# Performance work log

Hardware: AMD Instinct MI355X
Metric: run time of the kernel (lower is better)

Reference implementation:

```python
import jax, jax.numpy as jnp
import numpy as np

HIDDEN = 1024
HEADS = 16
HEAD_DIM = HIDDEN // HEADS
SCALE = HEAD_DIM ** (-0.5)


def setup_inputs() -> dict:
    key = jax.random.key(0)
    ks = jax.random.split(key, 5)
    B, N, C = 8, 1024, HIDDEN
    x = jax.random.normal(ks[0], (B, N, C), dtype=jnp.float32)
    # torch nn.Linear params: weight [out, in], bias [out]
    w_in = jax.random.normal(ks[1], (3 * C, C), dtype=jnp.float32) * (C ** -0.5)
    b_in = jax.random.normal(ks[2], (3 * C,), dtype=jnp.float32) * 0.02
    w_out = jax.random.normal(ks[3], (C, C), dtype=jnp.float32) * (C ** -0.5)
    b_out = jax.random.normal(ks[4], (C,), dtype=jnp.float32) * 0.02
    return {"x": x, "w_in": w_in, "b_in": b_in, "w_out": w_out, "b_out": b_out}


def reference(x, w_in, b_in, w_out, b_out):
    B, N, C = x.shape
    H, D = HEADS, HEAD_DIM
    # in_proj: [B,N,3C] -> (3,B,H,N,D)
    qkv = x @ w_in.T + b_in
    qkv = qkv.reshape(B, N, 3, H, D).transpose(2, 0, 3, 1, 4)
    q, k, v = qkv[0], qkv[1], qkv[2]
    # attention scores scaled after QK^T (same math as scaling q)
    attn = jnp.einsum("bhnd,bhmd->bhnm", q, k) * SCALE
    attn = jax.nn.softmax(attn, axis=-1)
    out = jnp.einsum("bhnm,bhmd->bhnd", attn, v)  # [B,H,N,D]
    out = out.transpose(0, 2, 1, 3).reshape(B, N, C)
    return out @ w_out.T + b_out
```

## Files before the change

kernel.cpp:

```cpp
#include <hip/hip_runtime.h>


typedef __attribute__((ext_vector_type(8))) __bf16 bf16x8;
typedef __attribute__((ext_vector_type(4))) __bf16 bf16x4;
typedef __attribute__((ext_vector_type(4))) float f32x4;
typedef __attribute__((ext_vector_type(4))) short short4v;

__device__ __forceinline__ f32x4 mfma16(bf16x8 a, bf16x8 b, f32x4 c) {
  return __builtin_amdgcn_mfma_f32_16x16x32_bf16(a, b, c, 0, 0, 0);
}

#if __has_builtin(__builtin_amdgcn_mfma_f32_16x16x16bf16_1k)
__device__ __forceinline__ f32x4 mfma_pv(bf16x4 a, bf16x4 b, f32x4 c) {
  short4v as = __builtin_bit_cast(short4v, a);
  short4v bs = __builtin_bit_cast(short4v, b);
  return __builtin_amdgcn_mfma_f32_16x16x16bf16_1k(as, bs, c, 0, 0, 0);
}
#else
__device__ __forceinline__ f32x4 mfma_pv(bf16x4 a, bf16x4 b, f32x4 c) {
  __bf16 z = (__bf16)0.f;
  bf16x8 a8 = {a[0], a[1], a[2], a[3], z, z, z, z};
  bf16x8 b8 = {b[0], b[1], b[2], b[3], z, z, z, z};
  return mfma16(a8, b8, c);
}
#endif

__device__ __forceinline__ float fexp2(float x) {
#if __has_builtin(__builtin_amdgcn_exp2f)
  return __builtin_amdgcn_exp2f(x);
#else
  return exp2f(x);
#endif
}

typedef __attribute__((address_space(1))) const unsigned int gu32;
typedef __attribute__((address_space(3))) unsigned int lu32;

__device__ __forceinline__ void async16(const void* g, void* l) {
  __builtin_amdgcn_global_load_lds((gu32*)g, (lu32*)l, 16, 0, 0);
}

__global__ __launch_bounds__(256) void cvt_all(const float* __restrict__ x,
                                               __bf16* __restrict__ xb,
                                               const float* __restrict__ wi,
                                               __bf16* __restrict__ wib,
                                               const float* __restrict__ wo,
                                               __bf16* __restrict__ wob) {
  int blk = blockIdx.x;
  const float* in;
  __bf16* out;
  int base;
  if (blk < 4096)      { in = x;  out = xb;  base = 0; }
  else if (blk < 5632) { in = wi; out = wib; base = 4096; }
  else                 { in = wo; out = wob; base = 5632; }
  int i = ((blk - base) * 256 + threadIdx.x) * 8;
  float4 a = *(const float4*)(in + i);
  float4 b = *(const float4*)(in + i + 4);
  bf16x8 o;
  o[0] = (__bf16)a.x; o[1] = (__bf16)a.y; o[2] = (__bf16)a.z; o[3] = (__bf16)a.w;
  o[4] = (__bf16)b.x; o[5] = (__bf16)b.y; o[6] = (__bf16)b.z; o[7] = (__bf16)b.w;
  *(bf16x8*)(out + i) = o;
}

template <bool WRITE_VT>
__global__ __launch_bounds__(512, 4) void gemm1(const __bf16* __restrict__ A,
                                                const __bf16* __restrict__ Bm,
                                                const float* __restrict__ bias,
                                                __bf16* __restrict__ C,
                                                __bf16* __restrict__ vt) {
  __shared__ char lds[49152];
  const int t = threadIdx.x;
  const int wv = t >> 6, lane = t & 63;
  const int q16 = lane & 15, quad = lane >> 4;
  const int wm = wv >> 1, wn = wv & 1;
  const int bid = blockIdx.x;
  const long m0 = (long)(bid & 31) * 256;
  const long n0 = (long)(bid >> 5) * 128;

  const int sr4 = t >> 2;
  const int gc = (t & 3) ^ ((sr4 >> 1) & 3);
  const int ldst = wv * 1024;

  const __bf16* srcA0 = A + (m0 + sr4) * 1024 + gc * 8;
  const __bf16* srcA1 = A + (m0 + 128 + sr4) * 1024 + gc * 8;
  const __bf16* srcB  = Bm + (n0 + sr4) * 1024 + gc * 8;

  const int raB = (wm * 64 + q16) * 64 + ((quad ^ ((q16 >> 1) & 3)) * 16);
  const int rbB = (wn * 64 + q16) * 64 + ((quad ^ ((q16 >> 1) & 3)) * 16);

  f32x4 zero = {0.f, 0.f, 0.f, 0.f};
  f32x4 acc[4][4];
#pragma unroll
  for (int i = 0; i < 4; ++i)
#pragma unroll
    for (int j = 0; j < 4; ++j) acc[i][j] = zero;

  async16(srcA0, lds + ldst);
  async16(srcA1, lds + 8192 + ldst);
  async16(srcB, lds + 16384 + ldst);
  __syncthreads();

  int cur = 0;
#pragma unroll 1
  for (int t32 = 0; t32 < 32; ++t32) {
    char* Ac = lds + cur * 24576;
    char* Bc = Ac + 16384;

    if (t32 < 31) {
      char* S = lds + (cur ^ 1) * 24576;
      const int kt = (t32 + 1) * 32;
      async16(srcA0 + kt, S + ldst);
      async16(srcA1 + kt, S + 8192 + ldst);
      async16(srcB + kt, S + 16384 + ldst);
    }

    bf16x8 af[4], bfr[4];
#pragma unroll
    for (int mi = 0; mi < 4; ++mi)
      af[mi] = *(const bf16x8*)(Ac + raB + mi * 1024);
#pragma unroll
    for (int nj = 0; nj < 4; ++nj)
      bfr[nj] = *(const bf16x8*)(Bc + rbB + nj * 1024);

    __builtin_amdgcn_s_setprio(1);
#pragma unroll
    for (int mi = 0; mi < 4; ++mi)
#pragma unroll
      for (int nj = 0; nj < 4; ++nj)
        acc[mi][nj] = mfma16(af[mi], bfr[nj], acc[mi][nj]);
    __builtin_amdgcn_s_setprio(0);

    __syncthreads();
    cur ^= 1;
  }

  if (WRITE_VT && n0 >= 2048) {
    const int b = (int)(m0 >> 10);
    const int nbase = (int)(m0 & 1023) + wm * 64;
#pragma unroll
    for (int nj = 0; nj < 4; ++nj) {
      int col = (int)n0 + wn * 64 + nj * 16 + q16;
      int cc = col - 2048;
      int h = cc >> 6, d = cc & 63;
      float bs = bias[col];
      __bf16* vrow = vt + (((long)(b * 16 + h)) << 16) + (long)d * 1024;
#pragma unroll
      for (int mi = 0; mi < 4; ++mi) {
        int n = nbase + mi * 16 + quad * 4;
        bf16x4 o;
#pragma unroll
        for (int r = 0; r < 4; ++r) o[r] = (__bf16)(acc[mi][nj][r] + bs);
        *(bf16x4*)(vrow + n) = o;
      }
    }
  } else {
#pragma unroll
    for (int nj = 0; nj < 4; ++nj) {
      long col = n0 + wn * 64 + nj * 16 + q16;
      float bs = bias[col];
#pragma unroll
      for (int mi = 0; mi < 4; ++mi) {
        long rowb = m0 + wm * 64 + mi * 16 + quad * 4;
#pragma unroll
        for (int r = 0; r < 4; ++r) {
          float v = acc[mi][nj][r] + bs;
          C[(rowb + r) * 3072 + col] = (__bf16)v;
        }
      }
    }
  }
}

__global__ __launch_bounds__(256, 4) void gemm2(const __bf16* __restrict__ A,
                                                const __bf16* __restrict__ Bm,
                                                const float* __restrict__ bias,
                                                float* __restrict__ C) {
  __shared__ char lds[32768];
  const int t = threadIdx.x;
  const int wv = t >> 6, lane = t & 63;
  const int q16 = lane & 15, quad = lane >> 4;
  const int wm = wv >> 1, wn = wv & 1;
  const long m0 = (long)blockIdx.x * 128;
  const long n0 = (long)blockIdx.y * 128;

  const int sr4 = t >> 2;
  const int gc = (t & 3) ^ ((sr4 >> 1) & 3);
  const int ldst = wv * 1024;

  const __bf16* srcA0 = A + (m0 + sr4) * 1024 + gc * 8;
  const __bf16* srcA1 = A + (m0 + 64 + sr4) * 1024 + gc * 8;
  const __bf16* srcB0 = Bm + (n0 + sr4) * 1024 + gc * 8;
  const __bf16* srcB1 = Bm + (n0 + 64 + sr4) * 1024 + gc * 8;

  const int raB = (wm * 64 + q16) * 64 + ((quad ^ ((q16 >> 1) & 3)) * 16);
  const int rbB = (wn * 64 + q16) * 64 + ((quad ^ ((q16 >> 1) & 3)) * 16);

  f32x4 zero = {0.f, 0.f, 0.f, 0.f};
  f32x4 acc[4][4];
#pragma unroll
  for (int i = 0; i < 4; ++i)
#pragma unroll
    for (int j = 0; j < 4; ++j) acc[i][j] = zero;

  async16(srcA0, lds + ldst);
  async16(srcA1, lds + 4096 + ldst);
  async16(srcB0, lds + 8192 + ldst);
  async16(srcB1, lds + 12288 + ldst);
  __syncthreads();

  int cur = 0;
#pragma unroll 1
  for (int t32 = 0; t32 < 32; ++t32) {
    char* Ac = lds + cur * 16384;
    char* Bc = Ac + 8192;

    if (t32 < 31) {
      char* S = lds + (cur ^ 1) * 16384;
      const int kt = (t32 + 1) * 32;
      async16(srcA0 + kt, S + ldst);
      async16(srcA1 + kt, S + 4096 + ldst);
      async16(srcB0 + kt, S + 8192 + ldst);
      async16(srcB1 + kt, S + 12288 + ldst);
    }

    bf16x8 af[4], bfr[4];
#pragma unroll
    for (int mi = 0; mi < 4; ++mi)
      af[mi] = *(const bf16x8*)(Ac + raB + mi * 1024);
#pragma unroll
    for (int nj = 0; nj < 4; ++nj)
      bfr[nj] = *(const bf16x8*)(Bc + rbB + nj * 1024);

    __builtin_amdgcn_s_setprio(1);
#pragma unroll
    for (int mi = 0; mi < 4; ++mi)
#pragma unroll
      for (int nj = 0; nj < 4; ++nj)
        acc[mi][nj] = mfma16(af[mi], bfr[nj], acc[mi][nj]);
    __builtin_amdgcn_s_setprio(0);

    __syncthreads();
    cur ^= 1;
  }

#pragma unroll
  for (int nj = 0; nj < 4; ++nj) {
    long col = n0 + wn * 64 + nj * 16 + q16;
    float bs = bias[col];
#pragma unroll
    for (int mi = 0; mi < 4; ++mi) {
      long rowb = m0 + wm * 64 + mi * 16 + quad * 4;
#pragma unroll
      for (int r = 0; r < 4; ++r) {
        float v = acc[mi][nj][r] + bs;
        C[(rowb + r) * 1024 + col] = v;
      }
    }
  }
}

__global__ __launch_bounds__(256) void attn_kernel(const __bf16* __restrict__ qkv,
                                                   const __bf16* __restrict__ vt,
                                                   __bf16* __restrict__ ao) {
  __shared__ __bf16 Ks[64 * 64];
  __shared__ __bf16 Vt[64 * 64];
  const int t = threadIdx.x;
  const int wv = t >> 6, lane = t & 63;
  const int q16 = lane & 15, quad = lane >> 4;
  const int bh = blockIdx.x;
  const int b = bh >> 4, h = bh & 15;
  const int q0 = blockIdx.y * 64;
  const long rowbase = (long)b * 1024;

  bf16x8 qf0, qf1;
  {
    long qrow = rowbase + q0 + wv * 16 + q16;
    const __bf16* qp = qkv + qrow * 3072 + h * 64 + quad * 8;
    qf0 = *(const bf16x8*)qp;
    qf1 = *(const bf16x8*)(qp + 32);
#pragma unroll
    for (int j = 0; j < 8; ++j) {
      qf0[j] = (__bf16)((float)qf0[j] * 0.18033688f);
      qf1[j] = (__bf16)((float)qf1[j] * 0.18033688f);
    }
  }

  f32x4 zero = {0.f, 0.f, 0.f, 0.f};
  f32x4 oacc[4];
#pragma unroll
  for (int dt = 0; dt < 4; ++dt) oacc[dt] = zero;
  float lcol = 0.f;

  char* KsB = (char*)Ks;
  char* VtB = (char*)Vt;
  const int sr = t >> 3;
  const int sgc = (t & 7) ^ (sr & 7);
  const int sw = q16 & 7;

  for (int kv0 = 0; kv0 < 1024; kv0 += 64) {
    __syncthreads();
    const __bf16* kg = qkv + (rowbase + kv0 + sr) * 3072 + 1024 + h * 64 + sgc * 8;
    async16(kg, KsB + wv * 1024);
    async16(kg + (long)32 * 3072, KsB + 4096 + wv * 1024);
    const __bf16* vg = vt + (long)bh * 65536 + (long)sr * 1024 + kv0 + sgc * 8;
    async16(vg, VtB + wv * 1024);
    async16(vg + (long)32 * 1024, VtB + 4096 + wv * 1024);
    __syncthreads();

    f32x4 sacc[4];
#pragma unroll
    for (int nt = 0; nt < 4; ++nt) sacc[nt] = zero;
#pragma unroll
    for (int nt = 0; nt < 4; ++nt) {
      int kvr = nt * 16 + q16;
      bf16x8 kf0 = *(const bf16x8*)(KsB + kvr * 128 + ((quad ^ sw) * 16));
      bf16x8 kf1 = *(const bf16x8*)(KsB + kvr * 128 + (((4 + quad) ^ sw) * 16));
      sacc[nt] = mfma16(kf0, qf0, sacc[nt]);
      sacc[nt] = mfma16(kf1, qf1, sacc[nt]);
    }

    bf16x4 pf[4];
#pragma unroll
    for (int nt = 0; nt < 4; ++nt)
#pragma unroll
      for (int r = 0; r < 4; ++r) {
        float p = fexp2(sacc[nt][r]);
        lcol += p;
        pf[nt][r] = (__bf16)p;
      }

#pragma unroll
    for (int nt = 0; nt < 4; ++nt) {
      int c = ((nt * 2 + (quad >> 1)) ^ sw) * 16 + (quad & 1) * 8;
#pragma unroll
      for (int dt = 0; dt < 4; ++dt) {
        bf16x4 vf = *(const bf16x4*)(VtB + (dt * 16 + q16) * 128 + c);
        oacc[dt] = mfma_pv(pf[nt], vf, oacc[dt]);
      }
    }
  }

  lcol += __shfl_xor(lcol, 16);
  lcol += __shfl_xor(lcol, 32);
  float inv = 1.0f / lcol;
#pragma unroll
  for (int r = 0; r < 4; ++r) {
    float ir = __shfl(inv, quad * 4 + r);
    long orow = rowbase + q0 + wv * 16 + quad * 4 + r;
#pragma unroll
    for (int dt = 0; dt < 4; ++dt)
      ao[orow * 1024 + h * 64 + dt * 16 + q16] = (__bf16)(oacc[dt][r] * ir);
  }
}

extern "C" void kernel_launch(void* const* d_in, const int* in_sizes, int n_in,
                              void* d_out, int out_size, void* d_ws, size_t ws_size,
                              hipStream_t stream) {
  const float* x     = (const float*)d_in[0];
  const float* w_in  = (const float*)d_in[1];
  const float* b_in  = (const float*)d_in[2];
  const float* w_out = (const float*)d_in[3];
  const float* b_out = (const float*)d_in[4];
  float* out = (float*)d_out;

  char* ws = (char*)d_ws;
  __bf16* xb   = (__bf16*)(ws);
  __bf16* wib  = (__bf16*)(ws + 16777216);
  __bf16* wob  = (__bf16*)(ws + 23068672);
  __bf16* qkvb = (__bf16*)(ws + 25165824);
  __bf16* aob  = (__bf16*)(ws + 75497472);
  __bf16* vtg  = (__bf16*)d_out;

  cvt_all<<<6144, 256, 0, stream>>>(x, xb, w_in, wib, w_out, wob);
  gemm1<true><<<768, 512, 0, stream>>>(xb, wib, b_in, qkvb, vtg);
  attn_kernel<<<dim3(128, 16), 256, 0, stream>>>(qkvb, vtg, aob);
  gemm2<<<dim3(64, 8), 256, 0, stream>>>(aob, wob, b_out, out);
}
```

Baseline: 237.6 us.

## Double-buffer attention KV tiles and shrink out-projection GEMM M-tile

The attention kernel moves from a single-buffered 64-row K/V tile, loaded between two barriers, to a double-buffered 32-row tile. The next tile's async loads now overlap the current tile's QK and PV MFMAs, leaving one barrier per iteration. The output-projection GEMM cuts its M tile from 128 to 64 rows, doubling its grid to 1024 blocks for better CU occupancy. The cost is more loop iterations with smaller MFMA batches and less operand reuse per block.

New measurement: 242.3 us. Within noise of the previous version (+2.0%).

```diff
diff --git a/kernel.cpp b/kernel.cpp
--- a/kernel.cpp
+++ b/kernel.cpp
@@ -175,57 +175,54 @@
                                                 const __bf16* __restrict__ Bm,
                                                 const float* __restrict__ bias,
                                                 float* __restrict__ C) {
-  __shared__ char lds[32768];
+  __shared__ char lds[24576];
   const int t = threadIdx.x;
   const int wv = t >> 6, lane = t & 63;
   const int q16 = lane & 15, quad = lane >> 4;
   const int wm = wv >> 1, wn = wv & 1;
-  const long m0 = (long)blockIdx.x * 128;
+  const long m0 = (long)blockIdx.x * 64;
   const long n0 = (long)blockIdx.y * 128;
 
-  const int sr4 = t >> 2;
-  const int gc = (t & 3) ^ ((sr4 >> 1) & 3);
+  const int sr2 = t >> 2;
+  const int gc = (t & 3) ^ ((sr2 >> 1) & 3);
   const int ldst = wv * 1024;
 
-  const __bf16* srcA0 = A + (m0 + sr4) * 1024 + gc * 8;
-  const __bf16* srcA1 = A + (m0 + 64 + sr4) * 1024 + gc * 8;
-  const __bf16* srcB0 = Bm + (n0 + sr4) * 1024 + gc * 8;
-  const __bf16* srcB1 = Bm + (n0 + 64 + sr4) * 1024 + gc * 8;
-
-  const int raB = (wm * 64 + q16) * 64 + ((quad ^ ((q16 >> 1) & 3)) * 16);
+  const __bf16* srcA  = A + (m0 + sr2) * 1024 + gc * 8;
+  const __bf16* srcB0 = Bm + (n0 + sr2) * 1024 + gc * 8;
+  const __bf16* srcB1 = Bm + (n0 + 64 + sr2) * 1024 + gc * 8;
+
+  const int raB = (wm * 32 + q16) * 64 + ((quad ^ ((q16 >> 1) & 3)) * 16);
   const int rbB = (wn * 64 + q16) * 64 + ((quad ^ ((q16 >> 1) & 3)) * 16);
 
   f32x4 zero = {0.f, 0.f, 0.f, 0.f};
-  f32x4 acc[4][4];
-#pragma unroll
-  for (int i = 0; i < 4; ++i)
+  f32x4 acc[2][4];
+#pragma unroll
+  for (int i = 0; i < 2; ++i)
 #pragma unroll
     for (int j = 0; j < 4; ++j) acc[i][j] = zero;
 
-  async16(srcA0, lds + ldst);
-  async16(srcA1, lds + 4096 + ldst);
-  async16(srcB0, lds + 8192 + ldst);
-  async16(srcB1, lds + 12288 + ldst);
+  async16(srcA, lds + ldst);
+  async16(srcB0, lds + 4096 + ldst);
+  async16(srcB1, lds + 8192 + ldst);
   __syncthreads();
 
   int cur = 0;
 #pragma unroll 1
   for (int t32 = 0; t32 < 32; ++t32) {
-    char* Ac = lds + cur * 16384;
-    char* Bc = Ac + 8192;
+    char* Ac = lds + cur * 12288;
+    char* Bc = Ac + 4096;
 
     if (t32 < 31) {
-      char* S = lds + (cur ^ 1) * 16384;
+      char* S = lds + (cur ^ 1) * 12288;
       const int kt = (t32 + 1) * 32;
-      async16(srcA0 + kt, S + ldst);
-      async16(srcA1 + kt, S + 4096 + ldst);
-      async16(srcB0 + kt, S + 8192 + ldst);
-      async16(srcB1 + kt, S + 12288 + ldst);
-    }
-
-    bf16x8 af[4], bfr[4];
-#pragma unroll
-    for (int mi = 0; mi < 4; ++mi)
+      async16(srcA + kt, S + ldst);
+      async16(srcB0 + kt, S + 4096 + ldst);
+      async16(srcB1 + kt, S + 8192 + ldst);
+    }
+
+    bf16x8 af[2], bfr[4];
+#pragma unroll
+    for (int mi = 0; mi < 2; ++mi)
       af[mi] = *(const bf16x8*)(Ac + raB + mi * 1024);
 #pragma unroll
     for (int nj = 0; nj < 4; ++nj)
@@ -233,7 +230,7 @@
 
     __builtin_amdgcn_s_setprio(1);
 #pragma unroll
-    for (int mi = 0; mi < 4; ++mi)
+    for (int mi = 0; mi < 2; ++mi)
 #pragma unroll
       for (int nj = 0; nj < 4; ++nj)
         acc[mi][nj] = mfma16(af[mi], bfr[nj], acc[mi][nj]);
@@ -248,8 +245,8 @@
     long col = n0 + wn * 64 + nj * 16 + q16;
     float bs = bias[col];
 #pragma unroll
-    for (int mi = 0; mi < 4; ++mi) {
-      long rowb = m0 + wm * 64 + mi * 16 + quad * 4;
+    for (int mi = 0; mi < 2; ++mi) {
+      long rowb = m0 + wm * 32 + mi * 16 + quad * 4;
 #pragma unroll
       for (int r = 0; r < 4; ++r) {
         float v = acc[mi][nj][r] + bs;
@@ -262,8 +259,7 @@
 __global__ __launch_bounds__(256) void attn_kernel(const __bf16* __restrict__ qkv,
                                                    const __bf16* __restrict__ vt,
                                                    __bf16* __restrict__ ao) {
-  __shared__ __bf16 Ks[64 * 64];
-  __shared__ __bf16 Vt[64 * 64];
+  __shared__ char lds[16384];
   const int t = threadIdx.x;
   const int wv = t >> 6, lane = t & 63;
   const int q16 = lane & 15, quad = lane >> 4;
@@ -291,27 +287,39 @@
   for (int dt = 0; dt < 4; ++dt) oacc[dt] = zero;
   float lcol = 0.f;
 
-  char* KsB = (char*)Ks;
-  char* VtB = (char*)Vt;
-  const int sr = t >> 3;
-  const int sgc = (t & 7) ^ (sr & 7);
+  const int sr8 = t >> 3;
+  const int sgc8 = (t & 7) ^ (sr8 & 7);
+  const int sr2 = t >> 2;
+  const int gc4 = (t & 3) ^ ((sr2 >> 1) & 3);
+  const int ldst = wv * 1024;
+
+  const __bf16* kbase = qkv + (rowbase + sr8) * 3072 + 1024 + h * 64 + sgc8 * 8;
+  const __bf16* vbase = vt + (long)bh * 65536 + (long)sr2 * 1024 + gc4 * 8;
+
   const int sw = q16 & 7;
-
-  for (int kv0 = 0; kv0 < 1024; kv0 += 64) {
-    __syncthreads();
-    const __bf16* kg = qkv + (rowbase + kv0 + sr) * 3072 + 1024 + h * 64 + sgc * 8;
-    async16(kg, KsB + wv * 1024);
-    async16(kg + (long)32 * 3072, KsB + 4096 + wv * 1024);
-    const __bf16* vg = vt + (long)bh * 65536 + (long)sr * 1024 + kv0 + sgc * 8;
-    async16(vg, VtB + wv * 1024);
-    async16(vg + (long)32 * 1024, VtB + 4096 + wv * 1024);
-    __syncthreads();
-
-    f32x4 sacc[4];
-#pragma unroll
-    for (int nt = 0; nt < 4; ++nt) sacc[nt] = zero;
-#pragma unroll
-    for (int nt = 0; nt < 4; ++nt) {
+  const int vg = (q16 >> 1) & 3;
+
+  async16(kbase, lds + ldst);
+  async16(vbase, lds + 8192 + ldst);
+  __syncthreads();
+
+  int cur = 0;
+#pragma unroll 1
+  for (int it = 0; it < 32; ++it) {
+    char* KsB = lds + cur * 4096;
+    char* VtB = lds + 8192 + cur * 4096;
+
+    if (it < 31) {
+      const int kv = (it + 1) * 32;
+      async16(kbase + (long)kv * 3072, lds + (cur ^ 1) * 4096 + ldst);
+      async16(vbase + kv, lds + 8192 + (cur ^ 1) * 4096 + ldst);
+    }
+
+    f32x4 sacc[2];
+#pragma unroll
+    for (int nt = 0; nt < 2; ++nt) sacc[nt] = zero;
+#pragma unroll
+    for (int nt = 0; nt < 2; ++nt) {
       int kvr = nt * 16 + q16;
       bf16x8 kf0 = *(const bf16x8*)(KsB + kvr * 128 + ((quad ^ sw) * 16));
       bf16x8 kf1 = *(const bf16x8*)(KsB + kvr * 128 + (((4 + quad) ^ sw) * 16));
@@ -319,9 +327,9 @@
       sacc[nt] = mfma16(kf1, qf1, sacc[nt]);
     }
 
-    bf16x4 pf[4];
-#pragma unroll
-    for (int nt = 0; nt < 4; ++nt)
+    bf16x4 pf[2];
+#pragma unroll
+    for (int nt = 0; nt < 2; ++nt)
 #pragma unroll
       for (int r = 0; r < 4; ++r) {
         float p = fexp2(sacc[nt][r]);
@@ -330,14 +338,17 @@
       }
 
 #pragma unroll
-    for (int nt = 0; nt < 4; ++nt) {
-      int c = ((nt * 2 + (quad >> 1)) ^ sw) * 16 + (quad & 1) * 8;
+    for (int nt = 0; nt < 2; ++nt) {
+      int c = (((nt * 2 + (quad >> 1)) ^ vg) * 16) + (quad & 1) * 8;
 #pragma unroll
       for (int dt = 0; dt < 4; ++dt) {
-        bf16x4 vf = *(const bf16x4*)(VtB + (dt * 16 + q16) * 128 + c);
+        bf16x4 vf = *(const bf16x4*)(VtB + (dt * 16 + q16) * 64 + c);
         oacc[dt] = mfma_pv(pf[nt], vf, oacc[dt]);
       }
     }
+
+    __syncthreads();
+    cur ^= 1;
   }
 
   lcol += __shfl_xor(lcol, 16);
@@ -374,5 +385,5 @@
   cvt_all<<<6144, 256, 0, stream>>>(x, xb, w_in, wib, w_out, wob);
   gemm1<true><<<768, 512, 0, stream>>>(xb, wib, b_in, qkvb, vtg);
   attn_kernel<<<dim3(128, 16), 256, 0, stream>>>(qkvb, vtg, aob);
-  gemm2<<<dim3(64, 8), 256, 0, stream>>>(aob, wob, b_out, out);
-}
+  gemm2<<<dim3(128, 8), 256, 0, stream>>>(aob, wob, b_out, out);
+}
```
